# Kernel optimization log

Hardware: AMD Instinct MI355X
Metric: run time of the kernel (lower is better)

Reference implementation:

```python
import jax, jax.numpy as jnp
import numpy as np

EPS = 1e-12  # torch F.normalize default eps
COMMITMENT_COST = 0.25

def l2_normalize(v, axis=-1):
    # matches torch.nn.functional.normalize(p=2): v / max(||v||, eps)
    n = jnp.linalg.norm(v, axis=axis, keepdims=True)
    return v / jnp.maximum(n, EPS)

def setup_inputs() -> dict:
    key = jax.random.key(0)
    k1, k2 = jax.random.split(key)
    N, D, K = 262144, 64, 1024
    x = jax.random.normal(k1, (N, D), dtype=jnp.float32)
    emb_weight = jax.random.normal(k2, (K, D), dtype=jnp.float32)
    return {"x": x, "emb_weight": emb_weight}

def reference(x, emb_weight):
    # x: [N, D] latents, emb_weight: [K, D] codebook
    xn = l2_normalize(x, axis=-1)                      # F.normalize(x, dim=-1)
    wn = l2_normalize(emb_weight, axis=-1)             # normalized codebook rows
    d2 = (jnp.sum(xn * xn, axis=-1, keepdims=True)
          + jnp.sum(wn * wn, axis=1)
          - 2.0 * jnp.matmul(xn, wn.T))                # [N, K]
    encoding_indices = jnp.argmin(d2, axis=1)          # [N]
    # quantize: normalize(embeddings(idx)) == wn[idx]
    quantized = wn[encoding_indices]                   # [N, D]
    q_latent_loss = jnp.mean((quantized - jax.lax.stop_gradient(xn)) ** 2)
    e_latent_loss = jnp.mean((xn - jax.lax.stop_gradient(quantized)) ** 2)
    loss = q_latent_loss + COMMITMENT_COST * e_latent_loss
    # straight-through estimator
    quantized_st = xn + jax.lax.stop_gradient(quantized - xn)
    return quantized_st, loss, encoding_indices
```

## Files before the change

### kernel.cpp

```cpp
#include <hip/hip_runtime.h>
#include <math.h>

#define N_ROWS 262144
#define DIM 64
#define K_CODES 1024
#define NT 32
#define ROWS_PER_BLOCK 128
#define EPSF 1e-12f

typedef _Float16 f16x8 __attribute__((ext_vector_type(8)));
typedef float f32x16 __attribute__((ext_vector_type(16)));


__global__ __launch_bounds__(64) void prep_codebook(
    const float* __restrict__ w, float* __restrict__ wn,
    float* __restrict__ msw, _Float16* __restrict__ wf)
{
    int k = blockIdx.x;
    int d = threadIdx.x;
    float v = w[k * DIM + d];
    float sq = v * v;
    #pragma unroll
    for (int off = 32; off; off >>= 1) sq += __shfl_xor(sq, off, 64);
    float n = fmaxf(sqrtf(sq), EPSF);
    float o = v / n;
    wn[k * DIM + d] = o;
    float s2 = o * o;
    #pragma unroll
    for (int off = 32; off; off >>= 1) s2 += __shfl_xor(s2, off, 64);
    if (d == 0) msw[k] = -0.5f * s2;

    _Float16 hi = (_Float16)o;
    _Float16 lo = (_Float16)(o - (float)hi);
    int t = k >> 5, nn = k & 31, s = d >> 4, g = (d >> 3) & 1, i = d & 7;
    size_t base = (size_t)t * 4096 + (size_t)s * 512 + (size_t)(g * 32 + nn) * 8 + i;
    wf[base] = hi;
    wf[base + 2048] = lo;
}

#define BODY(T, CW0, CW1, NL0, NL1)                                           \
  {                                                                           \
    const int cur = (T) & 1;                                                  \
    const _Float16* bp = &bbuf[cur][lane * 8];                                \
    f16x8 bh0 = *(const f16x8*)(bp);                                          \
    f16x8 bh1 = *(const f16x8*)(bp + 512);                                    \
    f16x8 bh2 = *(const f16x8*)(bp + 1024);                                   \
    f16x8 bh3 = *(const f16x8*)(bp + 1536);                                   \
    f16x8 bl0 = *(const f16x8*)(bp + 2048);                                   \
    f16x8 bl1 = *(const f16x8*)(bp + 2560);                                   \
    f16x8 bl2 = *(const f16x8*)(bp + 3072);                                   \
    f16x8 bl3 = *(const f16x8*)(bp + 3584);                                   \
    float mval = msw_lds[(T) * 32 + col];                                     \
    if ((T) + 1 < NT) {                                                       \
      *(f16x8*)&bbuf[cur ^ 1][tid * 16] = CW0;                                \
      *(f16x8*)&bbuf[cur ^ 1][tid * 16 + 8] = CW1;                            \
    }                                                                         \
    if ((T) + 2 < NT) {                                                       \
      NL0 = wf8[((T) + 2) * 512 + tid * 2];                                   \
      NL1 = wf8[((T) + 2) * 512 + tid * 2 + 1];                               \
    }                                                                         \
    f32x16 acc;                                                               \
    _Pragma("unroll")                                                         \
    for (int e = 0; e < 16; ++e) acc[e] = mval;                               \
    acc = __builtin_amdgcn_mfma_f32_32x32x16_f16(ah[0], bh0, acc, 0, 0, 0);   \
    acc = __builtin_amdgcn_mfma_f32_32x32x16_f16(ah[1], bh1, acc, 0, 0, 0);   \
    acc = __builtin_amdgcn_mfma_f32_32x32x16_f16(ah[2], bh2, acc, 0, 0, 0);   \
    acc = __builtin_amdgcn_mfma_f32_32x32x16_f16(ah[3], bh3, acc, 0, 0, 0);   \
    acc = __builtin_amdgcn_mfma_f32_32x32x16_f16(ah[0], bl0, acc, 0, 0, 0);   \
    acc = __builtin_amdgcn_mfma_f32_32x32x16_f16(ah[1], bl1, acc, 0, 0, 0);   \
    acc = __builtin_amdgcn_mfma_f32_32x32x16_f16(ah[2], bl2, acc, 0, 0, 0);   \
    acc = __builtin_amdgcn_mfma_f32_32x32x16_f16(ah[3], bl3, acc, 0, 0, 0);   \
    acc = __builtin_amdgcn_mfma_f32_32x32x16_f16(al[0], bh0, acc, 0, 0, 0);   \
    acc = __builtin_amdgcn_mfma_f32_32x32x16_f16(al[1], bh1, acc, 0, 0, 0);   \
    acc = __builtin_amdgcn_mfma_f32_32x32x16_f16(al[2], bh2, acc, 0, 0, 0);   \
    acc = __builtin_amdgcn_mfma_f32_32x32x16_f16(al[3], bh3, acc, 0, 0, 0);   \
    _Pragma("unroll")                                                         \
    for (int e = 0; e < 16; ++e)                                              \
      if (acc[e] > best[e]) { best[e] = acc[e]; bt[e] = (T); }                \
    __syncthreads();                                                          \
  }

__global__ __launch_bounds__(256, 3) void vq_main_kernel(
    const float* __restrict__ x,
    const float* __restrict__ wn,
    const float* __restrict__ msw,
    const _Float16* __restrict__ wf,
    float* __restrict__ out_q,
    float* __restrict__ out_idx,
    float* __restrict__ partial)
{
    __shared__ _Float16 bbuf[2][4096];
    __shared__ float msw_lds[K_CODES];
    __shared__ int idx_lds[ROWS_PER_BLOCK];
    __shared__ float inv_lds[ROWS_PER_BLOCK];
    __shared__ float red[4];

    const int tid = threadIdx.x;
    const int wv = tid >> 6;
    const int lane = tid & 63;
    const int col = lane & 31;
    const int g = lane >> 5;
    const int block_row0 = blockIdx.x * ROWS_PER_BLOCK;

    f16x8 ah[4], al[4];
    {
        const int arow = block_row0 + wv * 32 + col;
        const float* xrow = x + (size_t)arow * DIM + g * 8;
        float xv[4][8];
        #pragma unroll
        for (int s = 0; s < 4; ++s) {
            float4 q0 = *(const float4*)(xrow + s * 16);
            float4 q1 = *(const float4*)(xrow + s * 16 + 4);
            xv[s][0] = q0.x; xv[s][1] = q0.y; xv[s][2] = q0.z; xv[s][3] = q0.w;
            xv[s][4] = q1.x; xv[s][5] = q1.y; xv[s][6] = q1.z; xv[s][7] = q1.w;
        }
        float ss = 0.f;
        #pragma unroll
        for (int s = 0; s < 4; ++s)
            #pragma unroll
            for (int i = 0; i < 8; ++i) ss += xv[s][i] * xv[s][i];
        ss += __shfl_xor(ss, 32, 64);
        float nrm = fmaxf(sqrtf(ss), EPSF);
        float inv = 1.0f / nrm;
        if (g == 0) inv_lds[wv * 32 + col] = inv;
        #pragma unroll
        for (int s = 0; s < 4; ++s)
            #pragma unroll
            for (int i = 0; i < 8; ++i) {
                float v = xv[s][i] * inv;
                _Float16 hi = (_Float16)v;
                ah[s][i] = hi;
                al[s][i] = (_Float16)(v - (float)hi);
            }
    }

    {
        float4 mv = *(const float4*)(msw + tid * 4);
        *(float4*)&msw_lds[tid * 4] = mv;
    }

    const f16x8* wf8 = (const f16x8*)wf;
    f16x8 sA0, sA1, sB0, sB1;
    sB0 = wf8[tid * 2];
    sB1 = wf8[tid * 2 + 1];
    *(f16x8*)&bbuf[0][tid * 16] = sB0;
    *(f16x8*)&bbuf[0][tid * 16 + 8] = sB1;
    sA0 = wf8[512 + tid * 2];
    sA1 = wf8[512 + tid * 2 + 1];
    __syncthreads();

    float best[16];
    int bt[16];
    #pragma unroll
    for (int e = 0; e < 16; ++e) { best[e] = -3.4e38f; bt[e] = 0; }

    for (int tt = 0; tt < NT; tt += 2) {
        BODY(tt, sA0, sA1, sB0, sB1)
        BODY(tt + 1, sB0, sB1, sA0, sA1)
    }

    #pragma unroll
    for (int e = 0; e < 16; ++e) {
        float b = best[e];
        int bi = bt[e] * 32 + col;
        #pragma unroll
        for (int off = 1; off <= 16; off <<= 1) {
            float ob = __shfl_xor(b, off, 64);
            int oi = __shfl_xor(bi, off, 64);
            if (ob > b || (ob == b && oi < bi)) { b = ob; bi = oi; }
        }
        if (col == 0)
            idx_lds[wv * 32 + (e & 3) + 8 * (e >> 2) + 4 * g] = bi;
    }
    __syncthreads();

    const int lr = tid >> 1;
    const int grow = block_row0 + lr;
    const int d0 = (tid & 1) * 32;
    const int ci = idx_lds[lr];
    const float invn = inv_lds[lr];
    const float4* xp = (const float4*)(x + (size_t)grow * DIM + d0);
    const float4* qp = (const float4*)(wn + (size_t)ci * DIM + d0);
    float4* op = (float4*)(out_q + (size_t)grow * DIM + d0);
    float ls = 0.f;
    #pragma unroll
    for (int i = 0; i < 8; ++i) {
        float4 qv = qp[i];
        float4 xv4 = xp[i];
        float e0 = qv.x - xv4.x * invn;
        float e1 = qv.y - xv4.y * invn;
        float e2 = qv.z - xv4.z * invn;
        float e3 = qv.w - xv4.w * invn;
        ls += e0 * e0 + e1 * e1 + e2 * e2 + e3 * e3;
        op[i] = qv;
    }
    if (!(tid & 1)) out_idx[grow] = (float)ci;

    float s = ls;
    #pragma unroll
    for (int off = 32; off; off >>= 1) s += __shfl_xor(s, off, 64);
    if (lane == 0) red[wv] = s;
    __syncthreads();
    if (tid == 0) partial[blockIdx.x] = (red[0] + red[1]) + (red[2] + red[3]);
}

__global__ __launch_bounds__(256) void finalize_kernel(
    const float* __restrict__ partial, float* __restrict__ loss_out)
{
    __shared__ float red[4];
    int t = threadIdx.x;
    float s = 0.f;
    #pragma unroll
    for (int i = 0; i < 8; ++i) s += partial[t * 8 + i];
    #pragma unroll
    for (int off = 32; off; off >>= 1) s += __shfl_xor(s, off, 64);
    if ((t & 63) == 0) red[t >> 6] = s;
    __syncthreads();
    if (t == 0)
        *loss_out = 1.25f * (((red[0] + red[1]) + (red[2] + red[3]))
                             / (float)((size_t)N_ROWS * DIM));
}

extern "C" void kernel_launch(void* const* d_in, const int* in_sizes, int n_in,
                              void* d_out, int out_size, void* d_ws, size_t ws_size,
                              hipStream_t stream) {
    const float* x = (const float*)d_in[0];
    const float* w = (const float*)d_in[1];
    float* out = (float*)d_out;
    float* ws = (float*)d_ws;

    float* wn      = ws;
    float* msw     = wn + (size_t)K_CODES * DIM;
    float* partial = msw + K_CODES;
    _Float16* wf   = (_Float16*)(partial + 2048);

    float* out_q    = out;
    float* out_loss = out + (size_t)N_ROWS * DIM;
    float* out_idx  = out_loss + 1;

    prep_codebook<<<K_CODES, 64, 0, stream>>>(w, wn, msw, wf);
    vq_main_kernel<<<N_ROWS / ROWS_PER_BLOCK, 256, 0, stream>>>(
        x, wn, msw, wf, out_q, out_idx, partial);
    finalize_kernel<<<1, 256, 0, stream>>>(partial, out_loss);
}
```

Before: 136.3 us.

## Split MFMA chain into two accumulators and defer argmax compare by one tile

The 12-MFMA dependent chain per tile is split into two independent accumulator chains (hi and lo parts) so consecutive MFMAs can issue without waiting on each other. The argmax comparison for tile T is moved into the next iteration, where it can overlap with that tile's MFMAs. A final epilogue handles the last tile. The codebook staging loads and stores are also switched to contiguous per-thread indexing. This uses more registers for the second accumulator, which may hurt occupancy at 3 blocks per SM, and the changed summation order can shift results slightly.

New measurement: 280.0 us. 2.05x slower.

```diff
diff --git a/kernel.cpp b/kernel.cpp
--- a/kernel.cpp
+++ b/kernel.cpp
@@ -52,31 +52,35 @@
     f16x8 bl3 = *(const f16x8*)(bp + 3584);                                   \
     float mval = msw_lds[(T) * 32 + col];                                     \
     if ((T) + 1 < NT) {                                                       \
-      *(f16x8*)&bbuf[cur ^ 1][tid * 16] = CW0;                                \
-      *(f16x8*)&bbuf[cur ^ 1][tid * 16 + 8] = CW1;                            \
+      f16x8* wb = (f16x8*)&bbuf[cur ^ 1][0];                                  \
+      wb[tid] = CW0;                                                          \
+      wb[tid + 256] = CW1;                                                    \
     }                                                                         \
     if ((T) + 2 < NT) {                                                       \
-      NL0 = wf8[((T) + 2) * 512 + tid * 2];                                   \
-      NL1 = wf8[((T) + 2) * 512 + tid * 2 + 1];                               \
+      NL0 = wf8[((T) + 2) * 512 + tid];                                       \
+      NL1 = wf8[((T) + 2) * 512 + 256 + tid];                                 \
     }                                                                         \
-    f32x16 acc;                                                               \
+    if ((T) > 0) {                                                            \
+      _Pragma("unroll")                                                       \
+      for (int e = 0; e < 16; ++e) {                                          \
+        float s = acc0[e] + acc1[e];                                          \
+        if (s > best[e]) { best[e] = s; bt[e] = (T) - 1; }                    \
+      }                                                                       \
+    }                                                                         \
     _Pragma("unroll")                                                         \
-    for (int e = 0; e < 16; ++e) acc[e] = mval;                               \
-    acc = __builtin_amdgcn_mfma_f32_32x32x16_f16(ah[0], bh0, acc, 0, 0, 0);   \
-    acc = __builtin_amdgcn_mfma_f32_32x32x16_f16(ah[1], bh1, acc, 0, 0, 0);   \
-    acc = __builtin_amdgcn_mfma_f32_32x32x16_f16(ah[2], bh2, acc, 0, 0, 0);   \
-    acc = __builtin_amdgcn_mfma_f32_32x32x16_f16(ah[3], bh3, acc, 0, 0, 0);   \
-    acc = __builtin_amdgcn_mfma_f32_32x32x16_f16(ah[0], bl0, acc, 0, 0, 0);   \
-    acc = __builtin_amdgcn_mfma_f32_32x32x16_f16(ah[1], bl1, acc, 0, 0, 0);   \
-    acc = __builtin_amdgcn_mfma_f32_32x32x16_f16(ah[2], bl2, acc, 0, 0, 0);   \
-    acc = __builtin_amdgcn_mfma_f32_32x32x16_f16(ah[3], bl3, acc, 0, 0, 0);   \
-    acc = __builtin_amdgcn_mfma_f32_32x32x16_f16(al[0], bh0, acc, 0, 0, 0);   \
-    acc = __builtin_amdgcn_mfma_f32_32x32x16_f16(al[1], bh1, acc, 0, 0, 0);   \
-    acc = __builtin_amdgcn_mfma_f32_32x32x16_f16(al[2], bh2, acc, 0, 0, 0);   \
-    acc = __builtin_amdgcn_mfma_f32_32x32x16_f16(al[3], bh3, acc, 0, 0, 0);   \
-    _Pragma("unroll")                                                         \
-    for (int e = 0; e < 16; ++e)                                              \
-      if (acc[e] > best[e]) { best[e] = acc[e]; bt[e] = (T); }                \
+    for (int e = 0; e < 16; ++e) { acc0[e] = mval; acc1[e] = 0.f; }           \
+    acc0 = __builtin_amdgcn_mfma_f32_32x32x16_f16(ah[0], bh0, acc0, 0, 0, 0); \
+    acc1 = __builtin_amdgcn_mfma_f32_32x32x16_f16(ah[0], bl0, acc1, 0, 0, 0); \
+    acc0 = __builtin_amdgcn_mfma_f32_32x32x16_f16(ah[1], bh1, acc0, 0, 0, 0); \
+    acc1 = __builtin_amdgcn_mfma_f32_32x32x16_f16(ah[1], bl1, acc1, 0, 0, 0); \
+    acc0 = __builtin_amdgcn_mfma_f32_32x32x16_f16(ah[2], bh2, acc0, 0, 0, 0); \
+    acc1 = __builtin_amdgcn_mfma_f32_32x32x16_f16(ah[2], bl2, acc1, 0, 0, 0); \
+    acc0 = __builtin_amdgcn_mfma_f32_32x32x16_f16(ah[3], bh3, acc0, 0, 0, 0); \
+    acc1 = __builtin_amdgcn_mfma_f32_32x32x16_f16(ah[3], bl3, acc1, 0, 0, 0); \
+    acc0 = __builtin_amdgcn_mfma_f32_32x32x16_f16(al[0], bh0, acc0, 0, 0, 0); \
+    acc1 = __builtin_amdgcn_mfma_f32_32x32x16_f16(al[2], bh2, acc1, 0, 0, 0); \
+    acc0 = __builtin_amdgcn_mfma_f32_32x32x16_f16(al[1], bh1, acc0, 0, 0, 0); \
+    acc1 = __builtin_amdgcn_mfma_f32_32x32x16_f16(al[3], bh3, acc1, 0, 0, 0); \
     __syncthreads();                                                          \
   }
 
@@ -141,22 +145,31 @@
 
     const f16x8* wf8 = (const f16x8*)wf;
     f16x8 sA0, sA1, sB0, sB1;
-    sB0 = wf8[tid * 2];
-    sB1 = wf8[tid * 2 + 1];
-    *(f16x8*)&bbuf[0][tid * 16] = sB0;
-    *(f16x8*)&bbuf[0][tid * 16 + 8] = sB1;
-    sA0 = wf8[512 + tid * 2];
-    sA1 = wf8[512 + tid * 2 + 1];
+    sB0 = wf8[tid];
+    sB1 = wf8[256 + tid];
+    {
+        f16x8* wb = (f16x8*)&bbuf[0][0];
+        wb[tid] = sB0;
+        wb[tid + 256] = sB1;
+    }
+    sA0 = wf8[512 + tid];
+    sA1 = wf8[512 + 256 + tid];
     __syncthreads();
 
     float best[16];
     int bt[16];
     #pragma unroll
     for (int e = 0; e < 16; ++e) { best[e] = -3.4e38f; bt[e] = 0; }
+    f32x16 acc0, acc1;
 
     for (int tt = 0; tt < NT; tt += 2) {
         BODY(tt, sA0, sA1, sB0, sB1)
         BODY(tt + 1, sB0, sB1, sA0, sA1)
+    }
+    #pragma unroll
+    for (int e = 0; e < 16; ++e) {
+        float s = acc0[e] + acc1[e];
+        if (s > best[e]) { best[e] = s; bt[e] = NT - 1; }
     }
 
     #pragma unroll
```

## Switch to 16x16x32 MFMA with register-resident codebook tiles, dropping LDS staging

Applied to the files above, without the earlier changes.

Replaces the LDS double-buffered 32x32 MFMA loop with 16x16x32 MFMAs. Each wave now covers 64 rows as four row tiles and reuses each codebook fragment across them. Codebook fragments and bias terms are loaded straight from global memory one tile ahead, so the per-tile `__syncthreads` and LDS traffic go away. The codebook is re-laid out in 16-code tiles and blocks now handle 256 rows. The trade-offs are reliance on L1/L2 hits for the shared codebook reads and more accumulator/fragment registers per wave. The final prefetch iteration also reads past the end of the codebook buffer, and those values are never used.

Measured after the change: 163.3 us. 1.2x slower.

```diff
diff --git a/kernel.cpp b/kernel.cpp
--- a/kernel.cpp
+++ b/kernel.cpp
@@ -4,12 +4,12 @@
 #define N_ROWS 262144
 #define DIM 64
 #define K_CODES 1024
-#define NT 32
-#define ROWS_PER_BLOCK 128
+#define NT 64
+#define ROWS_PER_BLOCK 256
 #define EPSF 1e-12f
 
 typedef _Float16 f16x8 __attribute__((ext_vector_type(8)));
-typedef float f32x16 __attribute__((ext_vector_type(16)));
+typedef float f32x4 __attribute__((ext_vector_type(4)));
 
 
 __global__ __launch_bounds__(64) void prep_codebook(
@@ -32,53 +32,13 @@
 
     _Float16 hi = (_Float16)o;
     _Float16 lo = (_Float16)(o - (float)hi);
-    int t = k >> 5, nn = k & 31, s = d >> 4, g = (d >> 3) & 1, i = d & 7;
-    size_t base = (size_t)t * 4096 + (size_t)s * 512 + (size_t)(g * 32 + nn) * 8 + i;
+    int t = k >> 4, nn = k & 15;
+    int s = d >> 5, ks = d & 31, g = ks >> 3, i = ks & 7;
+    int lane = g * 16 + nn;
+    size_t base = (size_t)t * 2048 + (size_t)s * 512 + (size_t)lane * 8 + i;
     wf[base] = hi;
-    wf[base + 2048] = lo;
-}
-
-#define BODY(T, CW0, CW1, NL0, NL1)                                           \
-  {                                                                           \
-    const int cur = (T) & 1;                                                  \
-    const _Float16* bp = &bbuf[cur][lane * 8];                                \
-    f16x8 bh0 = *(const f16x8*)(bp);                                          \
-    f16x8 bh1 = *(const f16x8*)(bp + 512);                                    \
-    f16x8 bh2 = *(const f16x8*)(bp + 1024);                                   \
-    f16x8 bh3 = *(const f16x8*)(bp + 1536);                                   \
-    f16x8 bl0 = *(const f16x8*)(bp + 2048);                                   \
-    f16x8 bl1 = *(const f16x8*)(bp + 2560);                                   \
-    f16x8 bl2 = *(const f16x8*)(bp + 3072);                                   \
-    f16x8 bl3 = *(const f16x8*)(bp + 3584);                                   \
-    float mval = msw_lds[(T) * 32 + col];                                     \
-    if ((T) + 1 < NT) {                                                       \
-      *(f16x8*)&bbuf[cur ^ 1][tid * 16] = CW0;                                \
-      *(f16x8*)&bbuf[cur ^ 1][tid * 16 + 8] = CW1;                            \
-    }                                                                         \
-    if ((T) + 2 < NT) {                                                       \
-      NL0 = wf8[((T) + 2) * 512 + tid * 2];                                   \
-      NL1 = wf8[((T) + 2) * 512 + tid * 2 + 1];                               \
-    }                                                                         \
-    f32x16 acc;                                                               \
-    _Pragma("unroll")                                                         \
-    for (int e = 0; e < 16; ++e) acc[e] = mval;                               \
-    acc = __builtin_amdgcn_mfma_f32_32x32x16_f16(ah[0], bh0, acc, 0, 0, 0);   \
-    acc = __builtin_amdgcn_mfma_f32_32x32x16_f16(ah[1], bh1, acc, 0, 0, 0);   \
-    acc = __builtin_amdgcn_mfma_f32_32x32x16_f16(ah[2], bh2, acc, 0, 0, 0);   \
-    acc = __builtin_amdgcn_mfma_f32_32x32x16_f16(ah[3], bh3, acc, 0, 0, 0);   \
-    acc = __builtin_amdgcn_mfma_f32_32x32x16_f16(ah[0], bl0, acc, 0, 0, 0);   \
-    acc = __builtin_amdgcn_mfma_f32_32x32x16_f16(ah[1], bl1, acc, 0, 0, 0);   \
-    acc = __builtin_amdgcn_mfma_f32_32x32x16_f16(ah[2], bl2, acc, 0, 0, 0);   \
-    acc = __builtin_amdgcn_mfma_f32_32x32x16_f16(ah[3], bl3, acc, 0, 0, 0);   \
-    acc = __builtin_amdgcn_mfma_f32_32x32x16_f16(al[0], bh0, acc, 0, 0, 0);   \
-    acc = __builtin_amdgcn_mfma_f32_32x32x16_f16(al[1], bh1, acc, 0, 0, 0);   \
-    acc = __builtin_amdgcn_mfma_f32_32x32x16_f16(al[2], bh2, acc, 0, 0, 0);   \
-    acc = __builtin_amdgcn_mfma_f32_32x32x16_f16(al[3], bh3, acc, 0, 0, 0);   \
-    _Pragma("unroll")                                                         \
-    for (int e = 0; e < 16; ++e)                                              \
-      if (acc[e] > best[e]) { best[e] = acc[e]; bt[e] = (T); }                \
-    __syncthreads();                                                          \
-  }
+    wf[base + 1024] = lo;
+}
 
 __global__ __launch_bounds__(256, 3) void vq_main_kernel(
     const float* __restrict__ x,
@@ -89,8 +49,6 @@
     float* __restrict__ out_idx,
     float* __restrict__ partial)
 {
-    __shared__ _Float16 bbuf[2][4096];
-    __shared__ float msw_lds[K_CODES];
     __shared__ int idx_lds[ROWS_PER_BLOCK];
     __shared__ float inv_lds[ROWS_PER_BLOCK];
     __shared__ float red[4];
@@ -98,103 +56,141 @@
     const int tid = threadIdx.x;
     const int wv = tid >> 6;
     const int lane = tid & 63;
-    const int col = lane & 31;
-    const int g = lane >> 5;
+    const int nidx = lane & 15;
+    const int g = lane >> 4;
     const int block_row0 = blockIdx.x * ROWS_PER_BLOCK;
 
-    f16x8 ah[4], al[4];
-    {
-        const int arow = block_row0 + wv * 32 + col;
+    f16x8 ah[4][2], al[4][2];
+    #pragma unroll
+    for (int rt = 0; rt < 4; ++rt) {
+        const int arow = block_row0 + wv * 64 + rt * 16 + nidx;
         const float* xrow = x + (size_t)arow * DIM + g * 8;
-        float xv[4][8];
-        #pragma unroll
-        for (int s = 0; s < 4; ++s) {
-            float4 q0 = *(const float4*)(xrow + s * 16);
-            float4 q1 = *(const float4*)(xrow + s * 16 + 4);
+        float xv[2][8];
+        #pragma unroll
+        for (int s = 0; s < 2; ++s) {
+            float4 q0 = *(const float4*)(xrow + s * 32);
+            float4 q1 = *(const float4*)(xrow + s * 32 + 4);
             xv[s][0] = q0.x; xv[s][1] = q0.y; xv[s][2] = q0.z; xv[s][3] = q0.w;
             xv[s][4] = q1.x; xv[s][5] = q1.y; xv[s][6] = q1.z; xv[s][7] = q1.w;
         }
         float ss = 0.f;
         #pragma unroll
-        for (int s = 0; s < 4; ++s)
+        for (int s = 0; s < 2; ++s)
             #pragma unroll
             for (int i = 0; i < 8; ++i) ss += xv[s][i] * xv[s][i];
+        ss += __shfl_xor(ss, 16, 64);
         ss += __shfl_xor(ss, 32, 64);
         float nrm = fmaxf(sqrtf(ss), EPSF);
         float inv = 1.0f / nrm;
-        if (g == 0) inv_lds[wv * 32 + col] = inv;
-        #pragma unroll
-        for (int s = 0; s < 4; ++s)
+        if (g == 0) inv_lds[wv * 64 + rt * 16 + nidx] = inv;
+        #pragma unroll
+        for (int s = 0; s < 2; ++s)
             #pragma unroll
             for (int i = 0; i < 8; ++i) {
                 float v = xv[s][i] * inv;
                 _Float16 hi = (_Float16)v;
-                ah[s][i] = hi;
-                al[s][i] = (_Float16)(v - (float)hi);
+                ah[rt][s][i] = hi;
+                al[rt][s][i] = (_Float16)(v - (float)hi);
             }
     }
 
-    {
-        float4 mv = *(const float4*)(msw + tid * 4);
-        *(float4*)&msw_lds[tid * 4] = mv;
+    float best[4][4];
+    int bt[4][4];
+    #pragma unroll
+    for (int rt = 0; rt < 4; ++rt)
+        #pragma unroll
+        for (int r = 0; r < 4; ++r) { best[rt][r] = -3.4e38f; bt[rt][r] = 0; }
+
+    const f16x8* wf8 = (const f16x8*)wf;
+    f16x8 cb0 = wf8[lane];
+    f16x8 cb1 = wf8[64 + lane];
+    f16x8 cb2 = wf8[128 + lane];
+    f16x8 cb3 = wf8[192 + lane];
+    float mval = msw[nidx];
+
+    for (int t = 0; t < NT; ++t) {
+        const f16x8* np = wf8 + (size_t)(t + 1) * 256;
+        f16x8 nb0 = np[lane];
+        f16x8 nb1 = np[64 + lane];
+        f16x8 nb2 = np[128 + lane];
+        f16x8 nb3 = np[192 + lane];
+        float nmval = msw[(t + 1) * 16 + nidx];
+
+        f32x4 acc[4];
+        #pragma unroll
+        for (int rt = 0; rt < 4; ++rt) {
+            acc[rt][0] = mval; acc[rt][1] = mval;
+            acc[rt][2] = mval; acc[rt][3] = mval;
+        }
+        #pragma unroll
+        for (int rt = 0; rt < 4; ++rt)
+            acc[rt] = __builtin_amdgcn_mfma_f32_16x16x32_f16(ah[rt][0], cb0, acc[rt], 0, 0, 0);
+        #pragma unroll
+        for (int rt = 0; rt < 4; ++rt)
+            acc[rt] = __builtin_amdgcn_mfma_f32_16x16x32_f16(ah[rt][1], cb1, acc[rt], 0, 0, 0);
+        #pragma unroll
+        for (int rt = 0; rt < 4; ++rt)
+            acc[rt] = __builtin_amdgcn_mfma_f32_16x16x32_f16(al[rt][0], cb0, acc[rt], 0, 0, 0);
+        #pragma unroll
+        for (int rt = 0; rt < 4; ++rt)
+            acc[rt] = __builtin_amdgcn_mfma_f32_16x16x32_f16(al[rt][1], cb1, acc[rt], 0, 0, 0);
+        #pragma unroll
+        for (int rt = 0; rt < 4; ++rt)
+            acc[rt] = __builtin_amdgcn_mfma_f32_16x16x32_f16(ah[rt][0], cb2, acc[rt], 0, 0, 0);
+        #pragma unroll
+        for (int rt = 0; rt < 4; ++rt)
+            acc[rt] = __builtin_amdgcn_mfma_f32_16x16x32_f16(ah[rt][1], cb3, acc[rt], 0, 0, 0);
+
+        #pragma unroll
+        for (int rt = 0; rt < 4; ++rt)
+            #pragma unroll
+            for (int r = 0; r < 4; ++r)
+                if (acc[rt][r] > best[rt][r]) { best[rt][r] = acc[rt][r]; bt[rt][r] = t; }
+
+        cb0 = nb0; cb1 = nb1; cb2 = nb2; cb3 = nb3; mval = nmval;
     }
 
-    const f16x8* wf8 = (const f16x8*)wf;
-    f16x8 sA0, sA1, sB0, sB1;
-    sB0 = wf8[tid * 2];
-    sB1 = wf8[tid * 2 + 1];
-    *(f16x8*)&bbuf[0][tid * 16] = sB0;
-    *(f16x8*)&bbuf[0][tid * 16 + 8] = sB1;
-    sA0 = wf8[512 + tid * 2];
-    sA1 = wf8[512 + tid * 2 + 1];
+    #pragma unroll
+    for (int rt = 0; rt < 4; ++rt)
+        #pragma unroll
+        for (int r = 0; r < 4; ++r) {
+            float b = best[rt][r];
+            int bi = bt[rt][r] * 16 + nidx;
+            #pragma unroll
+            for (int off = 1; off <= 8; off <<= 1) {
+                float ob = __shfl_xor(b, off, 64);
+                int oi = __shfl_xor(bi, off, 64);
+                if (ob > b || (ob == b && oi < bi)) { b = ob; bi = oi; }
+            }
+            if (nidx == 0)
+                idx_lds[wv * 64 + rt * 16 + g * 4 + r] = bi;
+        }
     __syncthreads();
 
-    float best[16];
-    int bt[16];
-    #pragma unroll
-    for (int e = 0; e < 16; ++e) { best[e] = -3.4e38f; bt[e] = 0; }
-
-    for (int tt = 0; tt < NT; tt += 2) {
-        BODY(tt, sA0, sA1, sB0, sB1)
-        BODY(tt + 1, sB0, sB1, sA0, sA1)
+    float ls = 0.f;
+    #pragma unroll
+    for (int rep = 0; rep < 2; ++rep) {
+        const int lr = rep * 128 + (tid >> 1);
+        const int grow = block_row0 + lr;
+        const int d0 = (tid & 1) * 32;
+        const int ci = idx_lds[lr];
+        const float invn = inv_lds[lr];
+        const float4* xp = (const float4*)(x + (size_t)grow * DIM + d0);
+        const float4* qp = (const float4*)(wn + (size_t)ci * DIM + d0);
+        float4* op = (float4*)(out_q + (size_t)grow * DIM + d0);
+        #pragma unroll
+        for (int i = 0; i < 8; ++i) {
+            float4 qv = qp[i];
+            float4 xv4 = xp[i];
+            float e0 = qv.x - xv4.x * invn;
+            float e1 = qv.y - xv4.y * invn;
+            float e2 = qv.z - xv4.z * invn;
+            float e3 = qv.w - xv4.w * invn;
+            ls += e0 * e0 + e1 * e1 + e2 * e2 + e3 * e3;
+            op[i] = qv;
+        }
+        if (!(tid & 1)) out_idx[grow] = (float)ci;
     }
-
-    #pragma unroll
-    for (int e = 0; e < 16; ++e) {
-        float b = best[e];
-        int bi = bt[e] * 32 + col;
-        #pragma unroll
-        for (int off = 1; off <= 16; off <<= 1) {
-            float ob = __shfl_xor(b, off, 64);
-            int oi = __shfl_xor(bi, off, 64);
-            if (ob > b || (ob == b && oi < bi)) { b = ob; bi = oi; }
-        }
-        if (col == 0)
-            idx_lds[wv * 32 + (e & 3) + 8 * (e >> 2) + 4 * g] = bi;
-    }
-    __syncthreads();
-
-    const int lr = tid >> 1;
-    const int grow = block_row0 + lr;
-    const int d0 = (tid & 1) * 32;
-    const int ci = idx_lds[lr];
-    const float invn = inv_lds[lr];
-    const float4* xp = (const float4*)(x + (size_t)grow * DIM + d0);
-    const float4* qp = (const float4*)(wn + (size_t)ci * DIM + d0);
-    float4* op = (float4*)(out_q + (size_t)grow * DIM + d0);
-    float ls = 0.f;
-    #pragma unroll
-    for (int i = 0; i < 8; ++i) {
-        float4 qv = qp[i];
-        float4 xv4 = xp[i];
-        float e0 = qv.x - xv4.x * invn;
-        float e1 = qv.y - xv4.y * invn;
-        float e2 = qv.z - xv4.z * invn;
-        float e3 = qv.w - xv4.w * invn;
-        ls += e0 * e0 + e1 * e1 + e2 * e2 + e3 * e3;
-        op[i] = qv;
-    }
-    if (!(tid & 1)) out_idx[grow] = (float)ci;
 
     float s = ls;
     #pragma unroll
@@ -211,7 +207,7 @@
     int t = threadIdx.x;
     float s = 0.f;
     #pragma unroll
-    for (int i = 0; i < 8; ++i) s += partial[t * 8 + i];
+    for (int i = 0; i < 4; ++i) s += partial[t * 4 + i];
     #pragma unroll
     for (int off = 32; off; off >>= 1) s += __shfl_xor(s, off, 64);
     if ((t & 63) == 0) red[t >> 6] = s;
@@ -232,7 +228,7 @@
     float* wn      = ws;
     float* msw     = wn + (size_t)K_CODES * DIM;
     float* partial = msw + K_CODES;
-    _Float16* wf   = (_Float16*)(partial + 2048);
+    _Float16* wf   = (_Float16*)(partial + 1024);
 
     float* out_q    = out;
     float* out_loss = out + (size_t)N_ROWS * DIM;
```
